# Kernel optimization log

Hardware: AMD Instinct MI355X
Metric: run time of the kernel (lower is better)

Reference implementation:

```python
import jax, jax.numpy as jnp
import numpy as np

N_QUBITS = 4
NHEAD = 8


def _normalize_angles(v):
    # per-vector min/max scaling to [0, pi] over last axis (4 elems), as in torch code
    mn = v.min(axis=-1, keepdims=True)
    mx = v.max(axis=-1, keepdims=True)
    return (v - mn) / (mx - mn + 1e-8) * jnp.pi


def _apply_1q(state, U, w):
    # state: [B,H,S,S,2,2,2,2]; apply 2x2 complex gate U on wire w (axis 4+w)
    ax = 4 + w
    s = jnp.moveaxis(state, ax, -1)
    s = s @ U.T  # new[a] = sum_b U[a,b] old[b]
    return jnp.moveaxis(s, -1, ax)


def _apply_cnot(state, c, t):
    ca = 4 + c
    ta = 4 + t - (1 if t > c else 0)  # axis shift after take along ca
    s0 = jnp.take(state, 0, axis=ca)
    s1 = jnp.flip(jnp.take(state, 1, axis=ca), axis=ta)
    return jnp.stack([s0, s1], axis=ca)


def quantum_scores(qa, ka, params):
    # qa, ka: [B,H,S,4] angles in [0,pi]; params: [4]
    # PennyLane: RX(q_w) RZ(k_w) on |0> per wire -> product state, then RX(p_w); CNOT(w, w+1 mod 4); expval Z0
    qh = qa[:, :, :, None, :]  # [B,H,S,1,4] (row index i)
    kh = ka[:, :, None, :, :]  # [B,H,1,S,4] (col index j)
    c = jnp.cos(qh / 2)
    s = jnp.sin(qh / 2)
    amp0 = (c * jnp.exp(-0.5j * kh)).astype(jnp.complex64)   # [B,H,S,S,4]
    amp1 = (-1j * s * jnp.exp(0.5j * kh)).astype(jnp.complex64)
    w = jnp.stack([amp0, amp1], axis=-1)  # [B,H,S,S,4(wire),2(amp)]
    state = jnp.einsum('...a,...b,...c,...d->...abcd',
                       w[..., 0, :], w[..., 1, :], w[..., 2, :], w[..., 3, :])  # [B,H,S,S,2,2,2,2]
    for wq in range(N_QUBITS):
        th = params[wq]
        ct = jnp.cos(th / 2).astype(jnp.complex64)
        st = (-1j * jnp.sin(th / 2)).astype(jnp.complex64)
        U = jnp.stack([jnp.stack([ct, st]), jnp.stack([st, ct])])  # RX(theta)
        state = _apply_1q(state, U, wq)
        state = _apply_cnot(state, wq, (wq + 1) % N_QUBITS)
    probs = state.real ** 2 + state.imag ** 2  # [B,H,S,S,2,2,2,2]
    p = probs.sum(axis=(5, 6, 7))  # marginal over wires 1..3 -> [B,H,S,S,2]
    return p[..., 0] - p[..., 1]   # <Z_0>, [B,H,S,S]


def setup_inputs() -> dict:
    key = jax.random.key(0)
    ks = jax.random.split(key, 10)
    B, S, D = 4, 128, 256
    x = jax.random.normal(ks[0], (B, S, D), dtype=jnp.float32)
    def lin(k):
        kw, kb = jax.random.split(k)
        W = jax.random.normal(kw, (D, D), dtype=jnp.float32) * 0.05
        b = jax.random.normal(kb, (D,), dtype=jnp.float32) * 0.05
        return W, b
    Wq, bq = lin(ks[1]); Wk, bk = lin(ks[2]); Wv, bv = lin(ks[3]); Wo, bo = lin(ks[4])
    attn_params = jax.random.normal(ks[5], (N_QUBITS,), dtype=jnp.float32) * 0.1
    return {"x": x, "Wq": Wq, "bq": bq, "Wk": Wk, "bk": bk,
            "Wv": Wv, "bv": bv, "Wo": Wo, "bo": bo, "attn_params": attn_params}


def reference(x, Wq, bq, Wk, bk, Wv, bv, Wo, bo, attn_params):
    B, S, D = x.shape
    H = NHEAD
    dk = D // H
    Q = (x @ Wq.T + bq).reshape(B, S, H, dk)
    K = (x @ Wk.T + bk).reshape(B, S, H, dk)
    V = (x @ Wv.T + bv).reshape(B, S, H, dk)
    # angles from first n_qubits dims of each head, normalized per (b, i, h)
    qa = jnp.transpose(_normalize_angles(Q[..., :N_QUBITS]), (0, 2, 1, 3))  # [B,H,S,4]
    ka = jnp.transpose(_normalize_angles(K[..., :N_QUBITS]), (0, 2, 1, 3))  # [B,H,S,4]
    scores = quantum_scores(qa, ka, attn_params)  # [B,H,S,S]
    attn = jax.nn.softmax(scores / jnp.sqrt(jnp.float32(dk)), axis=-1)
    Vh = jnp.transpose(V, (0, 2, 1, 3))  # [B,H,S,dk]
    out = jnp.einsum('bhij,bhjd->bhid', attn, Vh)
    out = jnp.transpose(out, (0, 2, 1, 3)).reshape(B, S, D)
    return out @ Wo.T + bo
```

## Files before the change

### kernel.cpp

```cpp
#include <hip/hip_runtime.h>
#include <math.h>

namespace {

constexpr int kB  = 4;
constexpr int kS  = 128;
constexpr int kD  = 256;
constexpr int kH  = 8;
constexpr int kK  = 256;
constexpr float kPi    = 3.14159265358979323846f;
constexpr float kScale = 0.17677669529663687f;

typedef __bf16 bf16x8 __attribute__((ext_vector_type(8)));
typedef float  f32x4  __attribute__((ext_vector_type(4)));
typedef float  f32x8  __attribute__((ext_vector_type(8)));

__device__ inline void split8(const float* __restrict__ p, bf16x8& hi, bf16x8& lo) {
  const f32x8 v = *(const f32x8*)p;
#pragma unroll
  for (int e = 0; e < 8; ++e) {
    const __bf16 h = (__bf16)v[e];
    hi[e] = h;
    lo[e] = (__bf16)(v[e] - (float)h);
  }
}

__global__ void qkv_kernel(const float* __restrict__ x,
                           const float* __restrict__ Wq, const float* __restrict__ bq,
                           const float* __restrict__ Wk, const float* __restrict__ bk,
                           const float* __restrict__ Wv, const float* __restrict__ bv,
                           float* __restrict__ V, float* __restrict__ Qs,
                           float* __restrict__ Ks) {
  const int wave = threadIdx.x >> 6;
  const int lane = threadIdx.x & 63;
  const int ln = lane & 15;
  const int qd = lane >> 4;
  const int m0 = blockIdx.x * 16;
  const int ny = blockIdx.y;

  const float* W;
  const float* bias;
  int wrow;
  if (ny < 4) {
    W = Wv; bias = bv;
    wrow = ny * 64 + wave * 16 + ln;
  } else {
    const int c = (wave & 1) * 16 + ln;
    wrow = (c >> 2) * 32 + (c & 3);
    if (wave < 2) { W = Wq; bias = bq; } else { W = Wk; bias = bk; }
  }

  const float* ap = x + (m0 + ln) * kK + qd * 8;
  const float* bp = W + wrow * kK + qd * 8;

  f32x4 acc = {0.f, 0.f, 0.f, 0.f};
#pragma unroll
  for (int kc = 0; kc < kK; kc += 32) {
    bf16x8 Ah, Al, Bh, Bl;
    split8(ap + kc, Ah, Al);
    split8(bp + kc, Bh, Bl);
    acc = __builtin_amdgcn_mfma_f32_16x16x32_bf16(Ah, Bh, acc, 0, 0, 0);
    acc = __builtin_amdgcn_mfma_f32_16x16x32_bf16(Ah, Bl, acc, 0, 0, 0);
    acc = __builtin_amdgcn_mfma_f32_16x16x32_bf16(Al, Bh, acc, 0, 0, 0);
  }
  const float bvv = bias[wrow];
  const int row0 = m0 + qd * 4;
  if (ny < 4) {
    const int col = ny * 64 + wave * 16 + ln;
#pragma unroll
    for (int r = 0; r < 4; ++r)
      V[(row0 + r) * kD + col] = acc[r] + bvv;
  } else {
    const int c = (wave & 1) * 16 + ln;
    float* o = (wave < 2) ? Qs : Ks;
#pragma unroll
    for (int r = 0; r < 4; ++r)
      o[(row0 + r) * 32 + c] = acc[r] + bvv;
  }
}

__global__ void fused_attn_kernel(const float* __restrict__ Qs,
                                  const float* __restrict__ Ks,
                                  const float* __restrict__ V,
                                  const float* __restrict__ params,
                                  __bf16* __restrict__ aohi, __bf16* __restrict__ aolo) {
  __shared__ float kC[3][kS];
  __shared__ float Vl[kS][32];
  __shared__ float pl[16][kS + 4];
  __shared__ float qA[16][3], qB[16][3];

  const int bh = blockIdx.y;
  const int i0 = blockIdx.x * 16;
  const int b  = bh >> 3;
  const int h  = bh & 7;
  const int tid = threadIdx.x;

  if (tid < kS) {
    const float4 kv = *(const float4*)(Ks + (b * kS + tid) * 32 + h * 4);
    const float kmn = fminf(fminf(kv.x, kv.y), fminf(kv.z, kv.w));
    const float kmx = fmaxf(fmaxf(kv.x, kv.y), fmaxf(kv.z, kv.w));
    const float ksc = kPi / (kmx - kmn + 1e-8f);
    kC[0][tid] = cosf((kv.y - kmn) * ksc);
    kC[1][tid] = cosf((kv.z - kmn) * ksc);
    kC[2][tid] = cosf((kv.w - kmn) * ksc);
  } else if (tid < kS + 16) {
    const int il = tid - kS;
    const float4 qv = *(const float4*)(Qs + (b * kS + i0 + il) * 32 + h * 4);
    const float qmn = fminf(fminf(qv.x, qv.y), fminf(qv.z, qv.w));
    const float qmx = fmaxf(fmaxf(qv.x, qv.y), fmaxf(qv.z, qv.w));
    const float qsc = kPi / (qmx - qmn + 1e-8f);
    const float qn[3] = {(qv.y - qmn) * qsc, (qv.z - qmn) * qsc, (qv.w - qmn) * qsc};
#pragma unroll
    for (int w = 0; w < 3; ++w) {
      const float th = params[w + 1];
      qA[il][w] = cosf(th) * cosf(qn[w]);
      qB[il][w] = sinf(th) * sinf(qn[w]);
    }
  }
  {
    const int j0 = tid >> 5, d = tid & 31;
#pragma unroll
    for (int r = 0; r < 16; ++r) {
      const int j = r * 8 + j0;
      Vl[j][d] = V[(b * kS + j) * kD + h * 32 + d];
    }
  }
  __syncthreads();

  const int i_loc = tid >> 4;
  const int jl    = tid & 15;
  const float A1 = qA[i_loc][0], A2 = qA[i_loc][1], A3 = qA[i_loc][2];
  const float B1 = qB[i_loc][0], B2 = qB[i_loc][1], B3 = qB[i_loc][2];

  float e[8];
  float mx = -1e30f;
#pragma unroll
  for (int jj = 0; jj < 8; ++jj) {
    const int j = jl + 16 * jj;
    const float v = (A1 - B1 * kC[0][j]) * (A2 - B2 * kC[1][j]) *
                    (A3 - B3 * kC[2][j]) * kScale;
    e[jj] = v;
    mx = fmaxf(mx, v);
  }
#pragma unroll
  for (int m = 1; m < 16; m <<= 1) mx = fmaxf(mx, __shfl_xor(mx, m, 16));
  float sum = 0.f;
#pragma unroll
  for (int jj = 0; jj < 8; ++jj) { e[jj] = expf(e[jj] - mx); sum += e[jj]; }
#pragma unroll
  for (int m = 1; m < 16; m <<= 1) sum += __shfl_xor(sum, m, 16);
  const float inv = 1.f / sum;
#pragma unroll
  for (int jj = 0; jj < 8; ++jj) pl[i_loc][jl + 16 * jj] = e[jj] * inv;
  __syncthreads();

  const int d0 = tid & 15;
  float a0 = 0.f, a1 = 0.f;
#pragma unroll 4
  for (int j = 0; j < kS; ++j) {
    const float p = pl[i_loc][j];
    a0 = fmaf(p, Vl[j][d0], a0);
    a1 = fmaf(p, Vl[j][d0 + 16], a1);
  }
  const int base = (b * kS + i0 + i_loc) * kD + h * 32;
  const __bf16 h0 = (__bf16)a0;
  const __bf16 h1 = (__bf16)a1;
  aohi[base + d0]      = h0;
  aolo[base + d0]      = (__bf16)(a0 - (float)h0);
  aohi[base + d0 + 16] = h1;
  aolo[base + d0 + 16] = (__bf16)(a1 - (float)h1);
}

__global__ void out_gemm_kernel(const __bf16* __restrict__ aohi,
                                const __bf16* __restrict__ aolo,
                                const float* __restrict__ Wo,
                                const float* __restrict__ bo,
                                float* __restrict__ out) {
  const int wave = threadIdx.x >> 6;
  const int lane = threadIdx.x & 63;
  const int ln = lane & 15;
  const int qd = lane >> 4;
  const int m0 = blockIdx.x * 16;
  const int n0 = blockIdx.y * 64 + wave * 16;

  const __bf16* ap  = aohi + (m0 + ln) * kK + qd * 8;
  const __bf16* alp = aolo + (m0 + ln) * kK + qd * 8;
  const float*  bp  = Wo + (n0 + ln) * kK + qd * 8;

  f32x4 acc = {0.f, 0.f, 0.f, 0.f};
#pragma unroll
  for (int kc = 0; kc < kK; kc += 32) {
    const bf16x8 Ah = *(const bf16x8*)(ap  + kc);
    const bf16x8 Al = *(const bf16x8*)(alp + kc);
    bf16x8 Bh, Bl;
    split8(bp + kc, Bh, Bl);
    acc = __builtin_amdgcn_mfma_f32_16x16x32_bf16(Ah, Bh, acc, 0, 0, 0);
    acc = __builtin_amdgcn_mfma_f32_16x16x32_bf16(Ah, Bl, acc, 0, 0, 0);
    acc = __builtin_amdgcn_mfma_f32_16x16x32_bf16(Al, Bh, acc, 0, 0, 0);
  }
  const int col  = n0 + ln;
  const float bv = bo[col];
  const int row0 = m0 + qd * 4;
#pragma unroll
  for (int r = 0; r < 4; ++r)
    out[(row0 + r) * kD + col] = acc[r] + bv;
}

}

extern "C" void kernel_launch(void* const* d_in, const int* in_sizes, int n_in,
                              void* d_out, int out_size, void* d_ws, size_t ws_size,
                              hipStream_t stream) {
  const float* x  = (const float*)d_in[0];
  const float* Wq = (const float*)d_in[1];
  const float* bq = (const float*)d_in[2];
  const float* Wk = (const float*)d_in[3];
  const float* bk = (const float*)d_in[4];
  const float* Wv = (const float*)d_in[5];
  const float* bv = (const float*)d_in[6];
  const float* Wo = (const float*)d_in[7];
  const float* bo = (const float*)d_in[8];
  const float* pr = (const float*)d_in[9];
  float* out = (float*)d_out;

  float* ws = (float*)d_ws;
  float* V   = ws;
  float* Qs  = V + 131072;
  float* Ks  = Qs + 16384;
  __bf16* aohi = (__bf16*)(Ks + 16384);
  __bf16* aolo = aohi + 131072;

  qkv_kernel<<<dim3(32, 5), 256, 0, stream>>>(x, Wq, bq, Wk, bk, Wv, bv, V, Qs, Ks);
  fused_attn_kernel<<<dim3(8, 32), 256, 0, stream>>>(Qs, Ks, V, pr, aohi, aolo);
  out_gemm_kernel<<<dim3(32, 4), 256, 0, stream>>>(aohi, aolo, Wo, bo, out);
}
```

Baseline: 88.28 us.

## Fuse QKV, attention and output GEMM into one cooperative kernel with grid syncs

Merges the three kernels into a single persistent cooperative launch of 256 blocks that separates phases with grid-wide syncs. The QKV and output GEMM jobs are redistributed so each wave handles one 16x16 tile. This targets the launch overhead and inter-kernel gaps of three separate launches. In exchange it adds the cost of two grid barriers, the cooperative launch path, and lower parallelism in the GEMM phases, where only some waves have work.

```diff
diff --git a/kernel.cpp b/kernel.cpp
--- a/kernel.cpp
+++ b/kernel.cpp
@@ -1,5 +1,8 @@
 #include <hip/hip_runtime.h>
+#include <hip/hip_cooperative_groups.h>
 #include <math.h>
+
+namespace cg = cooperative_groups;
 
 namespace {
 
@@ -25,185 +28,196 @@
   }
 }
 
-__global__ void qkv_kernel(const float* __restrict__ x,
-                           const float* __restrict__ Wq, const float* __restrict__ bq,
-                           const float* __restrict__ Wk, const float* __restrict__ bk,
-                           const float* __restrict__ Wv, const float* __restrict__ bv,
-                           float* __restrict__ V, float* __restrict__ Qs,
-                           float* __restrict__ Ks) {
-  const int wave = threadIdx.x >> 6;
-  const int lane = threadIdx.x & 63;
-  const int ln = lane & 15;
-  const int qd = lane >> 4;
-  const int m0 = blockIdx.x * 16;
-  const int ny = blockIdx.y;
-
-  const float* W;
-  const float* bias;
-  int wrow;
-  if (ny < 4) {
-    W = Wv; bias = bv;
-    wrow = ny * 64 + wave * 16 + ln;
-  } else {
-    const int c = (wave & 1) * 16 + ln;
-    wrow = (c >> 2) * 32 + (c & 3);
-    if (wave < 2) { W = Wq; bias = bq; } else { W = Wk; bias = bk; }
-  }
-
-  const float* ap = x + (m0 + ln) * kK + qd * 8;
-  const float* bp = W + wrow * kK + qd * 8;
-
-  f32x4 acc = {0.f, 0.f, 0.f, 0.f};
-#pragma unroll
-  for (int kc = 0; kc < kK; kc += 32) {
-    bf16x8 Ah, Al, Bh, Bl;
-    split8(ap + kc, Ah, Al);
-    split8(bp + kc, Bh, Bl);
-    acc = __builtin_amdgcn_mfma_f32_16x16x32_bf16(Ah, Bh, acc, 0, 0, 0);
-    acc = __builtin_amdgcn_mfma_f32_16x16x32_bf16(Ah, Bl, acc, 0, 0, 0);
-    acc = __builtin_amdgcn_mfma_f32_16x16x32_bf16(Al, Bh, acc, 0, 0, 0);
-  }
-  const float bvv = bias[wrow];
-  const int row0 = m0 + qd * 4;
-  if (ny < 4) {
-    const int col = ny * 64 + wave * 16 + ln;
-#pragma unroll
-    for (int r = 0; r < 4; ++r)
-      V[(row0 + r) * kD + col] = acc[r] + bvv;
-  } else {
-    const int c = (wave & 1) * 16 + ln;
-    float* o = (wave < 2) ? Qs : Ks;
-#pragma unroll
-    for (int r = 0; r < 4; ++r)
-      o[(row0 + r) * 32 + c] = acc[r] + bvv;
-  }
-}
-
-__global__ void fused_attn_kernel(const float* __restrict__ Qs,
-                                  const float* __restrict__ Ks,
-                                  const float* __restrict__ V,
-                                  const float* __restrict__ params,
-                                  __bf16* __restrict__ aohi, __bf16* __restrict__ aolo) {
+__global__ void __launch_bounds__(256) fused_all(
+    const float* __restrict__ x,
+    const float* __restrict__ Wq, const float* __restrict__ bq,
+    const float* __restrict__ Wk, const float* __restrict__ bk,
+    const float* __restrict__ Wv, const float* __restrict__ bv,
+    const float* __restrict__ Wo, const float* __restrict__ bo,
+    const float* __restrict__ params,
+    float* __restrict__ V, float* __restrict__ Qs, float* __restrict__ Ks,
+    __bf16* __restrict__ aohi, __bf16* __restrict__ aolo,
+    float* __restrict__ out) {
   __shared__ float kC[3][kS];
   __shared__ float Vl[kS][32];
   __shared__ float pl[16][kS + 4];
   __shared__ float qA[16][3], qB[16][3];
 
-  const int bh = blockIdx.y;
-  const int i0 = blockIdx.x * 16;
-  const int b  = bh >> 3;
-  const int h  = bh & 7;
-  const int tid = threadIdx.x;
-
-  if (tid < kS) {
-    const float4 kv = *(const float4*)(Ks + (b * kS + tid) * 32 + h * 4);
-    const float kmn = fminf(fminf(kv.x, kv.y), fminf(kv.z, kv.w));
-    const float kmx = fmaxf(fmaxf(kv.x, kv.y), fmaxf(kv.z, kv.w));
-    const float ksc = kPi / (kmx - kmn + 1e-8f);
-    kC[0][tid] = cosf((kv.y - kmn) * ksc);
-    kC[1][tid] = cosf((kv.z - kmn) * ksc);
-    kC[2][tid] = cosf((kv.w - kmn) * ksc);
-  } else if (tid < kS + 16) {
-    const int il = tid - kS;
-    const float4 qv = *(const float4*)(Qs + (b * kS + i0 + il) * 32 + h * 4);
-    const float qmn = fminf(fminf(qv.x, qv.y), fminf(qv.z, qv.w));
-    const float qmx = fmaxf(fmaxf(qv.x, qv.y), fmaxf(qv.z, qv.w));
-    const float qsc = kPi / (qmx - qmn + 1e-8f);
-    const float qn[3] = {(qv.y - qmn) * qsc, (qv.z - qmn) * qsc, (qv.w - qmn) * qsc};
-#pragma unroll
-    for (int w = 0; w < 3; ++w) {
-      const float th = params[w + 1];
-      qA[il][w] = cosf(th) * cosf(qn[w]);
-      qB[il][w] = sinf(th) * sinf(qn[w]);
-    }
-  }
-  {
-    const int j0 = tid >> 5, d = tid & 31;
-#pragma unroll
-    for (int r = 0; r < 16; ++r) {
-      const int j = r * 8 + j0;
-      Vl[j][d] = V[(b * kS + j) * kD + h * 32 + d];
-    }
-  }
-  __syncthreads();
-
-  const int i_loc = tid >> 4;
-  const int jl    = tid & 15;
-  const float A1 = qA[i_loc][0], A2 = qA[i_loc][1], A3 = qA[i_loc][2];
-  const float B1 = qB[i_loc][0], B2 = qB[i_loc][1], B3 = qB[i_loc][2];
-
-  float e[8];
-  float mx = -1e30f;
-#pragma unroll
-  for (int jj = 0; jj < 8; ++jj) {
-    const int j = jl + 16 * jj;
-    const float v = (A1 - B1 * kC[0][j]) * (A2 - B2 * kC[1][j]) *
-                    (A3 - B3 * kC[2][j]) * kScale;
-    e[jj] = v;
-    mx = fmaxf(mx, v);
-  }
-#pragma unroll
-  for (int m = 1; m < 16; m <<= 1) mx = fmaxf(mx, __shfl_xor(mx, m, 16));
-  float sum = 0.f;
-#pragma unroll
-  for (int jj = 0; jj < 8; ++jj) { e[jj] = expf(e[jj] - mx); sum += e[jj]; }
-#pragma unroll
-  for (int m = 1; m < 16; m <<= 1) sum += __shfl_xor(sum, m, 16);
-  const float inv = 1.f / sum;
-#pragma unroll
-  for (int jj = 0; jj < 8; ++jj) pl[i_loc][jl + 16 * jj] = e[jj] * inv;
-  __syncthreads();
-
-  const int d0 = tid & 15;
-  float a0 = 0.f, a1 = 0.f;
-#pragma unroll 4
-  for (int j = 0; j < kS; ++j) {
-    const float p = pl[i_loc][j];
-    a0 = fmaf(p, Vl[j][d0], a0);
-    a1 = fmaf(p, Vl[j][d0 + 16], a1);
-  }
-  const int base = (b * kS + i0 + i_loc) * kD + h * 32;
-  const __bf16 h0 = (__bf16)a0;
-  const __bf16 h1 = (__bf16)a1;
-  aohi[base + d0]      = h0;
-  aolo[base + d0]      = (__bf16)(a0 - (float)h0);
-  aohi[base + d0 + 16] = h1;
-  aolo[base + d0 + 16] = (__bf16)(a1 - (float)h1);
-}
-
-__global__ void out_gemm_kernel(const __bf16* __restrict__ aohi,
-                                const __bf16* __restrict__ aolo,
-                                const float* __restrict__ Wo,
-                                const float* __restrict__ bo,
-                                float* __restrict__ out) {
-  const int wave = threadIdx.x >> 6;
-  const int lane = threadIdx.x & 63;
+  cg::grid_group grid = cg::this_grid();
+
+  const int tid  = threadIdx.x;
+  const int wave = tid >> 6;
+  const int lane = tid & 63;
   const int ln = lane & 15;
   const int qd = lane >> 4;
-  const int m0 = blockIdx.x * 16;
-  const int n0 = blockIdx.y * 64 + wave * 16;
-
-  const __bf16* ap  = aohi + (m0 + ln) * kK + qd * 8;
-  const __bf16* alp = aolo + (m0 + ln) * kK + qd * 8;
-  const float*  bp  = Wo + (n0 + ln) * kK + qd * 8;
-
-  f32x4 acc = {0.f, 0.f, 0.f, 0.f};
-#pragma unroll
-  for (int kc = 0; kc < kK; kc += 32) {
-    const bf16x8 Ah = *(const bf16x8*)(ap  + kc);
-    const bf16x8 Al = *(const bf16x8*)(alp + kc);
-    bf16x8 Bh, Bl;
-    split8(bp + kc, Bh, Bl);
-    acc = __builtin_amdgcn_mfma_f32_16x16x32_bf16(Ah, Bh, acc, 0, 0, 0);
-    acc = __builtin_amdgcn_mfma_f32_16x16x32_bf16(Ah, Bl, acc, 0, 0, 0);
-    acc = __builtin_amdgcn_mfma_f32_16x16x32_bf16(Al, Bh, acc, 0, 0, 0);
-  }
-  const int col  = n0 + ln;
-  const float bv = bo[col];
-  const int row0 = m0 + qd * 4;
-#pragma unroll
-  for (int r = 0; r < 4; ++r)
-    out[(row0 + r) * kD + col] = acc[r] + bv;
+  const int blockId = blockIdx.y * gridDim.x + blockIdx.x;
+
+  {
+    const int job = wave * 256 + blockId;
+    if (job < 640) {
+      const int mx  = job & 31;
+      const int seg = job >> 5;
+      const int ny  = seg >> 2;
+      const int w   = seg & 3;
+      const int m0  = mx * 16;
+
+      const float* W;
+      const float* bias;
+      int wrow;
+      if (ny < 4) {
+        W = Wv; bias = bv;
+        wrow = ny * 64 + w * 16 + ln;
+      } else {
+        const int c = (w & 1) * 16 + ln;
+        wrow = (c >> 2) * 32 + (c & 3);
+        if (w < 2) { W = Wq; bias = bq; } else { W = Wk; bias = bk; }
+      }
+
+      const float* ap = x + (m0 + ln) * kK + qd * 8;
+      const float* bp = W + wrow * kK + qd * 8;
+
+      f32x4 acc = {0.f, 0.f, 0.f, 0.f};
+#pragma unroll
+      for (int kc = 0; kc < kK; kc += 32) {
+        bf16x8 Ah, Al, Bh, Bl;
+        split8(ap + kc, Ah, Al);
+        split8(bp + kc, Bh, Bl);
+        acc = __builtin_amdgcn_mfma_f32_16x16x32_bf16(Ah, Bh, acc, 0, 0, 0);
+        acc = __builtin_amdgcn_mfma_f32_16x16x32_bf16(Ah, Bl, acc, 0, 0, 0);
+        acc = __builtin_amdgcn_mfma_f32_16x16x32_bf16(Al, Bh, acc, 0, 0, 0);
+      }
+      const float bvv = bias[wrow];
+      const int row0 = m0 + qd * 4;
+      if (ny < 4) {
+        const int col = ny * 64 + w * 16 + ln;
+#pragma unroll
+        for (int r = 0; r < 4; ++r)
+          V[(row0 + r) * kD + col] = acc[r] + bvv;
+      } else {
+        const int c = (w & 1) * 16 + ln;
+        float* o = (w < 2) ? Qs : Ks;
+#pragma unroll
+        for (int r = 0; r < 4; ++r)
+          o[(row0 + r) * 32 + c] = acc[r] + bvv;
+      }
+    }
+  }
+  grid.sync();
+
+  {
+    const int bh = blockIdx.y;
+    const int i0 = blockIdx.x * 16;
+    const int b  = bh >> 3;
+    const int h  = bh & 7;
+
+    if (tid < kS) {
+      const float4 kv = *(const float4*)(Ks + (b * kS + tid) * 32 + h * 4);
+      const float kmn = fminf(fminf(kv.x, kv.y), fminf(kv.z, kv.w));
+      const float kmx = fmaxf(fmaxf(kv.x, kv.y), fmaxf(kv.z, kv.w));
+      const float ksc = kPi / (kmx - kmn + 1e-8f);
+      kC[0][tid] = cosf((kv.y - kmn) * ksc);
+      kC[1][tid] = cosf((kv.z - kmn) * ksc);
+      kC[2][tid] = cosf((kv.w - kmn) * ksc);
+    } else if (tid < kS + 16) {
+      const int il = tid - kS;
+      const float4 qv = *(const float4*)(Qs + (b * kS + i0 + il) * 32 + h * 4);
+      const float qmn = fminf(fminf(qv.x, qv.y), fminf(qv.z, qv.w));
+      const float qmx = fmaxf(fmaxf(qv.x, qv.y), fmaxf(qv.z, qv.w));
+      const float qsc = kPi / (qmx - qmn + 1e-8f);
+      const float qn[3] = {(qv.y - qmn) * qsc, (qv.z - qmn) * qsc, (qv.w - qmn) * qsc};
+#pragma unroll
+      for (int w = 0; w < 3; ++w) {
+        const float th = params[w + 1];
+        qA[il][w] = cosf(th) * cosf(qn[w]);
+        qB[il][w] = sinf(th) * sinf(qn[w]);
+      }
+    }
+    {
+      const int j0 = tid >> 5, d = tid & 31;
+#pragma unroll
+      for (int r = 0; r < 16; ++r) {
+        const int j = r * 8 + j0;
+        Vl[j][d] = V[(b * kS + j) * kD + h * 32 + d];
+      }
+    }
+    __syncthreads();
+
+    const int i_loc = tid >> 4;
+    const int jl    = tid & 15;
+    const float A1 = qA[i_loc][0], A2 = qA[i_loc][1], A3 = qA[i_loc][2];
+    const float B1 = qB[i_loc][0], B2 = qB[i_loc][1], B3 = qB[i_loc][2];
+
+    float e[8];
+    float mx = -1e30f;
+#pragma unroll
+    for (int jj = 0; jj < 8; ++jj) {
+      const int j = jl + 16 * jj;
+      const float v = (A1 - B1 * kC[0][j]) * (A2 - B2 * kC[1][j]) *
+                      (A3 - B3 * kC[2][j]) * kScale;
+      e[jj] = v;
+      mx = fmaxf(mx, v);
+    }
+#pragma unroll
+    for (int m = 1; m < 16; m <<= 1) mx = fmaxf(mx, __shfl_xor(mx, m, 16));
+    float sum = 0.f;
+#pragma unroll
+    for (int jj = 0; jj < 8; ++jj) { e[jj] = expf(e[jj] - mx); sum += e[jj]; }
+#pragma unroll
+    for (int m = 1; m < 16; m <<= 1) sum += __shfl_xor(sum, m, 16);
+    const float inv = 1.f / sum;
+#pragma unroll
+    for (int jj = 0; jj < 8; ++jj) pl[i_loc][jl + 16 * jj] = e[jj] * inv;
+    __syncthreads();
+
+    const int d0 = tid & 15;
+    float a0 = 0.f, a1 = 0.f;
+#pragma unroll 4
+    for (int j = 0; j < kS; ++j) {
+      const float p = pl[i_loc][j];
+      a0 = fmaf(p, Vl[j][d0], a0);
+      a1 = fmaf(p, Vl[j][d0 + 16], a1);
+    }
+    const int base = (b * kS + i0 + i_loc) * kD + h * 32;
+    const __bf16 h0 = (__bf16)a0;
+    const __bf16 h1 = (__bf16)a1;
+    aohi[base + d0]      = h0;
+    aolo[base + d0]      = (__bf16)(a0 - (float)h0);
+    aohi[base + d0 + 16] = h1;
+    aolo[base + d0 + 16] = (__bf16)(a1 - (float)h1);
+  }
+  grid.sync();
+
+  {
+    const int job = wave * 256 + blockId;
+    if (job < 512) {
+      const int mx = job & 31;
+      const int ct = job >> 5;
+      const int m0 = mx * 16;
+      const int n0 = ct * 16;
+
+      const __bf16* ap  = aohi + (m0 + ln) * kK + qd * 8;
+      const __bf16* alp = aolo + (m0 + ln) * kK + qd * 8;
+      const float*  bp  = Wo + (n0 + ln) * kK + qd * 8;
+
+      f32x4 acc = {0.f, 0.f, 0.f, 0.f};
+#pragma unroll
+      for (int kc = 0; kc < kK; kc += 32) {
+        const bf16x8 Ah = *(const bf16x8*)(ap  + kc);
+        const bf16x8 Al = *(const bf16x8*)(alp + kc);
+        bf16x8 Bh, Bl;
+        split8(bp + kc, Bh, Bl);
+        acc = __builtin_amdgcn_mfma_f32_16x16x32_bf16(Ah, Bh, acc, 0, 0, 0);
+        acc = __builtin_amdgcn_mfma_f32_16x16x32_bf16(Ah, Bl, acc, 0, 0, 0);
+        acc = __builtin_amdgcn_mfma_f32_16x16x32_bf16(Al, Bh, acc, 0, 0, 0);
+      }
+      const int col  = n0 + ln;
+      const float bv = bo[col];
+      const int row0 = m0 + qd * 4;
+#pragma unroll
+      for (int r = 0; r < 4; ++r)
+        out[(row0 + r) * kD + col] = acc[r] + bv;
+    }
+  }
 }
 
 }
@@ -230,7 +244,10 @@
   __bf16* aohi = (__bf16*)(Ks + 16384);
   __bf16* aolo = aohi + 131072;
 
-  qkv_kernel<<<dim3(32, 5), 256, 0, stream>>>(x, Wq, bq, Wk, bk, Wv, bv, V, Qs, Ks);
-  fused_attn_kernel<<<dim3(8, 32), 256, 0, stream>>>(Qs, Ks, V, pr, aohi, aolo);
-  out_gemm_kernel<<<dim3(32, 4), 256, 0, stream>>>(aohi, aolo, Wo, bo, out);
-}
+  void* args[] = {(void*)&x,  (void*)&Wq, (void*)&bq, (void*)&Wk, (void*)&bk,
+                  (void*)&Wv, (void*)&bv, (void*)&Wo, (void*)&bo, (void*)&pr,
+                  (void*)&V,  (void*)&Qs, (void*)&Ks, (void*)&aohi, (void*)&aolo,
+                  (void*)&out};
+  hipLaunchCooperativeKernel((const void*)fused_all, dim3(8, 32), dim3(256, 1, 1),
+                             args, 0, stream);
+}
```

New measurement: 155.7 us. 76.4% more time.

## Fuse output projection into attention kernel using per-head atomic accumulation

Applied to the files above, without the earlier changes.

The separate output GEMM kernel is removed. Each attention block now multiplies its 16x32 head output tile by the matching 32-column slice of Wo with MFMA and accumulates into the output through atomic float adds, with bias added only by head 0. The output is zeroed with a memset beforehand. This saves a kernel launch and the bf16 hi/lo intermediate round trip, but adds a memset, eight-way atomic contention per output element, and order-dependent float summation.

```diff
diff --git a/kernel.cpp b/kernel.cpp
--- a/kernel.cpp
+++ b/kernel.cpp
@@ -3,10 +3,8 @@
 
 namespace {
 
-constexpr int kB  = 4;
 constexpr int kS  = 128;
 constexpr int kD  = 256;
-constexpr int kH  = 8;
 constexpr int kK  = 256;
 constexpr float kPi    = 3.14159265358979323846f;
 constexpr float kScale = 0.17677669529663687f;
@@ -79,21 +77,26 @@
   }
 }
 
-__global__ void fused_attn_kernel(const float* __restrict__ Qs,
-                                  const float* __restrict__ Ks,
-                                  const float* __restrict__ V,
-                                  const float* __restrict__ params,
-                                  __bf16* __restrict__ aohi, __bf16* __restrict__ aolo) {
+__global__ void __launch_bounds__(256) fused_attn_out(
+    const float* __restrict__ Qs, const float* __restrict__ Ks,
+    const float* __restrict__ V,  const float* __restrict__ params,
+    const float* __restrict__ Wo, const float* __restrict__ bo,
+    float* __restrict__ out) {
   __shared__ float kC[3][kS];
   __shared__ float Vl[kS][32];
   __shared__ float pl[16][kS + 4];
   __shared__ float qA[16][3], qB[16][3];
+  __shared__ float ao_l[16][36];
 
   const int bh = blockIdx.y;
   const int i0 = blockIdx.x * 16;
   const int b  = bh >> 3;
   const int h  = bh & 7;
   const int tid = threadIdx.x;
+  const int wave = tid >> 6;
+  const int lane = tid & 63;
+  const int ln = lane & 15;
+  const int qd = lane >> 4;
 
   if (tid < kS) {
     const float4 kv = *(const float4*)(Ks + (b * kS + tid) * 32 + h * 4);
@@ -129,81 +132,75 @@
 
   const int i_loc = tid >> 4;
   const int jl    = tid & 15;
-  const float A1 = qA[i_loc][0], A2 = qA[i_loc][1], A3 = qA[i_loc][2];
-  const float B1 = qB[i_loc][0], B2 = qB[i_loc][1], B3 = qB[i_loc][2];
-
-  float e[8];
-  float mx = -1e30f;
-#pragma unroll
-  for (int jj = 0; jj < 8; ++jj) {
-    const int j = jl + 16 * jj;
-    const float v = (A1 - B1 * kC[0][j]) * (A2 - B2 * kC[1][j]) *
-                    (A3 - B3 * kC[2][j]) * kScale;
-    e[jj] = v;
-    mx = fmaxf(mx, v);
-  }
-#pragma unroll
-  for (int m = 1; m < 16; m <<= 1) mx = fmaxf(mx, __shfl_xor(mx, m, 16));
-  float sum = 0.f;
-#pragma unroll
-  for (int jj = 0; jj < 8; ++jj) { e[jj] = expf(e[jj] - mx); sum += e[jj]; }
-#pragma unroll
-  for (int m = 1; m < 16; m <<= 1) sum += __shfl_xor(sum, m, 16);
-  const float inv = 1.f / sum;
-#pragma unroll
-  for (int jj = 0; jj < 8; ++jj) pl[i_loc][jl + 16 * jj] = e[jj] * inv;
+  {
+    const float A1 = qA[i_loc][0], A2 = qA[i_loc][1], A3 = qA[i_loc][2];
+    const float B1 = qB[i_loc][0], B2 = qB[i_loc][1], B3 = qB[i_loc][2];
+
+    float e[8];
+    float mx = -1e30f;
+#pragma unroll
+    for (int jj = 0; jj < 8; ++jj) {
+      const int j = jl + 16 * jj;
+      const float v = (A1 - B1 * kC[0][j]) * (A2 - B2 * kC[1][j]) *
+                      (A3 - B3 * kC[2][j]) * kScale;
+      e[jj] = v;
+      mx = fmaxf(mx, v);
+    }
+#pragma unroll
+    for (int m = 1; m < 16; m <<= 1) mx = fmaxf(mx, __shfl_xor(mx, m, 16));
+    float sum = 0.f;
+#pragma unroll
+    for (int jj = 0; jj < 8; ++jj) { e[jj] = expf(e[jj] - mx); sum += e[jj]; }
+#pragma unroll
+    for (int m = 1; m < 16; m <<= 1) sum += __shfl_xor(sum, m, 16);
+    const float inv = 1.f / sum;
+#pragma unroll
+    for (int jj = 0; jj < 8; ++jj) pl[i_loc][jl + 16 * jj] = e[jj] * inv;
+  }
   __syncthreads();
 
-  const int d0 = tid & 15;
-  float a0 = 0.f, a1 = 0.f;
+  {
+    const int d0 = jl;
+    float a0 = 0.f, a1 = 0.f;
 #pragma unroll 4
-  for (int j = 0; j < kS; ++j) {
-    const float p = pl[i_loc][j];
-    a0 = fmaf(p, Vl[j][d0], a0);
-    a1 = fmaf(p, Vl[j][d0 + 16], a1);
-  }
-  const int base = (b * kS + i0 + i_loc) * kD + h * 32;
-  const __bf16 h0 = (__bf16)a0;
-  const __bf16 h1 = (__bf16)a1;
-  aohi[base + d0]      = h0;
-  aolo[base + d0]      = (__bf16)(a0 - (float)h0);
-  aohi[base + d0 + 16] = h1;
-  aolo[base + d0 + 16] = (__bf16)(a1 - (float)h1);
-}
-
-__global__ void out_gemm_kernel(const __bf16* __restrict__ aohi,
-                                const __bf16* __restrict__ aolo,
-                                const float* __restrict__ Wo,
-                                const float* __restrict__ bo,
-                                float* __restrict__ out) {
-  const int wave = threadIdx.x >> 6;
-  const int lane = threadIdx.x & 63;
-  const int ln = lane & 15;
-  const int qd = lane >> 4;
-  const int m0 = blockIdx.x * 16;
-  const int n0 = blockIdx.y * 64 + wave * 16;
-
-  const __bf16* ap  = aohi + (m0 + ln) * kK + qd * 8;
-  const __bf16* alp = aolo + (m0 + ln) * kK + qd * 8;
-  const float*  bp  = Wo + (n0 + ln) * kK + qd * 8;
-
-  f32x4 acc = {0.f, 0.f, 0.f, 0.f};
-#pragma unroll
-  for (int kc = 0; kc < kK; kc += 32) {
-    const bf16x8 Ah = *(const bf16x8*)(ap  + kc);
-    const bf16x8 Al = *(const bf16x8*)(alp + kc);
-    bf16x8 Bh, Bl;
-    split8(bp + kc, Bh, Bl);
-    acc = __builtin_amdgcn_mfma_f32_16x16x32_bf16(Ah, Bh, acc, 0, 0, 0);
-    acc = __builtin_amdgcn_mfma_f32_16x16x32_bf16(Ah, Bl, acc, 0, 0, 0);
-    acc = __builtin_amdgcn_mfma_f32_16x16x32_bf16(Al, Bh, acc, 0, 0, 0);
-  }
-  const int col  = n0 + ln;
-  const float bv = bo[col];
-  const int row0 = m0 + qd * 4;
-#pragma unroll
-  for (int r = 0; r < 4; ++r)
-    out[(row0 + r) * kD + col] = acc[r] + bv;
+    for (int j = 0; j < kS; ++j) {
+      const float p = pl[i_loc][j];
+      a0 = fmaf(p, Vl[j][d0], a0);
+      a1 = fmaf(p, Vl[j][d0 + 16], a1);
+    }
+    ao_l[i_loc][d0]      = a0;
+    ao_l[i_loc][d0 + 16] = a1;
+  }
+  __syncthreads();
+
+  {
+    bf16x8 Ah, Al;
+#pragma unroll
+    for (int e = 0; e < 8; ++e) {
+      const float v = ao_l[ln][qd * 8 + e];
+      const __bf16 hi = (__bf16)v;
+      Ah[e] = hi;
+      Al[e] = (__bf16)(v - (float)hi);
+    }
+    const int row0 = b * kS + i0 + qd * 4;
+#pragma unroll
+    for (int q = 0; q < 4; ++q) {
+      const int col = wave * 64 + q * 16 + ln;
+      const float* bp = Wo + col * kK + h * 32 + qd * 8;
+      bf16x8 Bh, Bl;
+      split8(bp, Bh, Bl);
+      f32x4 acc = {0.f, 0.f, 0.f, 0.f};
+      acc = __builtin_amdgcn_mfma_f32_16x16x32_bf16(Ah, Bh, acc, 0, 0, 0);
+      acc = __builtin_amdgcn_mfma_f32_16x16x32_bf16(Ah, Bl, acc, 0, 0, 0);
+      acc = __builtin_amdgcn_mfma_f32_16x16x32_bf16(Al, Bh, acc, 0, 0, 0);
+      const float bias = (h == 0) ? bo[col] : 0.f;
+#pragma unroll
+      for (int r = 0; r < 4; ++r) {
+        __hip_atomic_fetch_add(&out[(row0 + r) * kD + col], acc[r] + bias,
+                               __ATOMIC_RELAXED, __HIP_MEMORY_SCOPE_AGENT);
+      }
+    }
+  }
 }
 
 }
@@ -227,10 +224,8 @@
   float* V   = ws;
   float* Qs  = V + 131072;
   float* Ks  = Qs + 16384;
-  __bf16* aohi = (__bf16*)(Ks + 16384);
-  __bf16* aolo = aohi + 131072;
-
+
+  hipMemsetAsync(out, 0, out_size, stream);
   qkv_kernel<<<dim3(32, 5), 256, 0, stream>>>(x, Wq, bq, Wk, bk, Wv, bv, V, Qs, Ks);
-  fused_attn_kernel<<<dim3(8, 32), 256, 0, stream>>>(Qs, Ks, V, pr, aohi, aolo);
-  out_gemm_kernel<<<dim3(32, 4), 256, 0, stream>>>(aohi, aolo, Wo, bo, out);
-}
+  fused_attn_out<<<dim3(8, 32), 256, 0, stream>>>(Qs, Ks, V, pr, Wo, bo, out);
+}
```

Result: no change. 87.56 us (-0.8%).
